# Kernel tuning notes

Measured on AMD Instinct MI355X. Metric: run time of the kernel, lower is better.

Reference implementation:

```python
import jax, jax.numpy as jnp
import numpy as np

B, S, D_IN, E, H, F, O = 32, 1024, 256, 512, 512, 2048, 512


def setup_inputs() -> dict:
    key = jax.random.key(0)
    ks = jax.random.split(key, 10)
    s = 0.02
    return {
        "x": jax.random.normal(ks[0], (B, S, D_IN), dtype=jnp.float32),
        "W_enc": jax.random.normal(ks[1], (D_IN, E), dtype=jnp.float32) * s,
        "b_enc": jnp.zeros((E,), dtype=jnp.float32),
        "W_ih": jax.random.normal(ks[2], (E, 4 * H), dtype=jnp.float32) * s,
        "W_hh": jax.random.normal(ks[3], (H, 4 * H), dtype=jnp.float32) * s,
        "b_lstm": jnp.zeros((4 * H,), dtype=jnp.float32),
        "W1": jax.random.normal(ks[4], (E, F), dtype=jnp.float32) * s,
        "b1": jnp.zeros((F,), dtype=jnp.float32),
        "W2": jax.random.normal(ks[5], (F, O), dtype=jnp.float32) * s,
        "b2": jnp.zeros((O,), dtype=jnp.float32),
    }


def _lstm(xs, W_ih, W_hh, b):
    # xs: [S, B, E] -> outputs [S, B, H], final (h, c) each [B, H]
    h0 = jnp.zeros((xs.shape[1], W_hh.shape[0]), dtype=xs.dtype)
    c0 = jnp.zeros_like(h0)

    def step(carry, x_t):
        h, c = carry
        z = x_t @ W_ih + h @ W_hh + b  # [B, 4H]
        i, f, g, o = jnp.split(z, 4, axis=-1)
        i = jax.nn.sigmoid(i)
        f = jax.nn.sigmoid(f)
        g = jnp.tanh(g)
        o = jax.nn.sigmoid(o)
        c = f * c + i * g
        h = o * jnp.tanh(c)
        return (h, c), h

    (h_n, c_n), ys = jax.lax.scan(step, (h0, c0), xs)
    return ys, h_n, c_n


def reference(x, W_enc, b_enc, W_ih, W_hh, b_lstm, W1, b1, W2, b2):
    # encoder: per-token linear projection, then permute to time-major
    embedded = x @ W_enc + b_enc              # [B, S, E]
    embedded = jnp.transpose(embedded, (1, 0, 2))  # [S, B, E]
    # decoder LSTM over the sequence dimension
    output, h_n, c_n = _lstm(embedded, W_ih, W_hh, b_lstm)
    # per-position 2-layer MLP (vectorized version of the (i,j) loop):
    # fc2(fc1(relu(embedded)))  -- note ReLU is applied BEFORE fc1, and no
    # nonlinearity between fc1 and fc2, matching the torch code.
    embed_out = (jax.nn.relu(embedded) @ W1 + b1) @ W2 + b2  # [S, B, O]
    return output, h_n[None], c_n[None], embed_out
```

## Files before the change

kernel.cpp:

```cpp
#include <hip/hip_runtime.h>
#include <hip/hip_bf16.h>
#include <stdint.h>

typedef uint16_t u16;
typedef uint32_t u32;
typedef unsigned long long u64;
typedef __attribute__((ext_vector_type(8))) short short8;
typedef __attribute__((ext_vector_type(4))) float f32x4;

#define NS 1024

__device__ __forceinline__ float bf2f(u16 v) {
  union { u32 u; float f; } x; x.u = ((u32)v) << 16; return x.f;
}
__device__ __forceinline__ u16 f2bf(float f) {
  union { float f; u32 u; } x; x.f = f;
  u32 r = x.u + 0x7FFFu + ((x.u >> 16) & 1u);
  return (u16)(r >> 16);
}
__device__ __forceinline__ u32 relu2bf(u32 x) {
  u32 kill = (((x >> 15) & 1u) * 0x0000FFFFu) | (((x >> 31) & 1u) * 0xFFFF0000u);
  return x & ~kill;
}
__device__ __forceinline__ f32x4 shfl_x4(f32x4 v, int m) {
  f32x4 r;
  r[0] = __shfl_xor(v[0], m); r[1] = __shfl_xor(v[1], m);
  r[2] = __shfl_xor(v[2], m); r[3] = __shfl_xor(v[3], m);
  return r;
}

__global__ __launch_bounds__(256) void k_cast(const float* __restrict__ in,
                                              u16* __restrict__ out, int n4) {
  int i = blockIdx.x * 256 + threadIdx.x;
  if (i >= n4) return;
  float4 v = ((const float4*)in)[i];
  ushort4 o;
  o.x = f2bf(v.x); o.y = f2bf(v.y); o.z = f2bf(v.z); o.w = f2bf(v.w);
  ((ushort4*)out)[i] = o;
}

__global__ __launch_bounds__(256) void k_transpose(const float* __restrict__ in,
                                                   u16* __restrict__ out,
                                                   int K, int N) {
  __shared__ u16 tile[32][33];
  int k0 = blockIdx.x * 32, n0 = blockIdx.y * 32;
  int tid = threadIdx.x;
#pragma unroll
  for (int i = 0; i < 4; i++) {
    int idx = i * 256 + tid;
    int r = idx >> 5, c = idx & 31;
    tile[r][c] = f2bf(in[(size_t)(k0 + r) * N + n0 + c]);
  }
  __syncthreads();
#pragma unroll
  for (int i = 0; i < 4; i++) {
    int idx = i * 256 + tid;
    int r = idx >> 5, c = idx & 31;
    out[(size_t)(n0 + r) * K + k0 + c] = tile[c][r];
  }
}

template <bool REMAP, bool RELU_A, bool OUTF32>
__global__ __launch_bounds__(256) void k_gemm(const u16* __restrict__ A,
                                              const u16* __restrict__ Bt,
                                              const float* __restrict__ bias,
                                              void* __restrict__ Cout,
                                              int M, int N, int K) {
  __shared__ u16 As[128 * 32];
  __shared__ u16 Bs[128 * 32];
  const int m0 = blockIdx.x * 128, n0 = blockIdx.y * 128;
  const int tid = threadIdx.x;
  const int wave = tid >> 6, lane = tid & 63;
  const int wm = wave >> 1, wn = wave & 1;
  f32x4 acc[4][4] = {};

  for (int kt = 0; kt < K; kt += 32) {
    uint4 av[2], bv[2];
#pragma unroll
    for (int i = 0; i < 2; i++) {
      int idx = i * 256 + tid;
      int r = idx >> 2, ch = idx & 3;
      av[i] = *(const uint4*)(A + (size_t)(m0 + r) * K + kt + ch * 8);
      bv[i] = *(const uint4*)(Bt + (size_t)(n0 + r) * K + kt + ch * 8);
      if (RELU_A) {
        u32* p = (u32*)&av[i];
        p[0] = relu2bf(p[0]); p[1] = relu2bf(p[1]);
        p[2] = relu2bf(p[2]); p[3] = relu2bf(p[3]);
      }
    }
    __syncthreads();
#pragma unroll
    for (int i = 0; i < 2; i++) {
      int idx = i * 256 + tid;
      int r = idx >> 2, ch = idx & 3;
      *(uint4*)(As + r * 32 + ch * 8) = av[i];
      *(uint4*)(Bs + r * 32 + ch * 8) = bv[i];
    }
    __syncthreads();
    short8 af[4], bf[4];
#pragma unroll
    for (int mi = 0; mi < 4; mi++) {
      int row = wm * 64 + mi * 16 + (lane & 15);
      af[mi] = *(const short8*)(As + row * 32 + (lane >> 4) * 8);
    }
#pragma unroll
    for (int ni = 0; ni < 4; ni++) {
      int col = wn * 64 + ni * 16 + (lane & 15);
      bf[ni] = *(const short8*)(Bs + col * 32 + (lane >> 4) * 8);
    }
#pragma unroll
    for (int mi = 0; mi < 4; mi++)
#pragma unroll
      for (int ni = 0; ni < 4; ni++)
        acc[mi][ni] = __builtin_amdgcn_mfma_f32_16x16x32_bf16(af[mi], bf[ni], acc[mi][ni], 0, 0, 0);
  }

#pragma unroll
  for (int mi = 0; mi < 4; mi++)
#pragma unroll
    for (int ni = 0; ni < 4; ni++) {
      int col = n0 + wn * 64 + ni * 16 + (lane & 15);
      float bvad = bias[col];
#pragma unroll
      for (int r = 0; r < 4; r++) {
        int row = m0 + wm * 64 + mi * 16 + (lane >> 4) * 4 + r;
        float v = acc[mi][ni][r] + bvad;
        size_t orow = REMAP ? ((size_t)(row & 1023) * 32 + (size_t)(row >> 10))
                            : (size_t)row;
        if (OUTF32) ((float*)Cout)[orow * N + col] = v;
        else        ((u16*)Cout)[orow * N + col] = f2bf(v);
      }
    }
}

__global__ __launch_bounds__(256, 1) void k_lstm(
    const u16* __restrict__ Whh_t,
    const u16* __restrict__ Wih_t,
    const u16* __restrict__ emb,
    const float* __restrict__ b_lstm,
    u64* __restrict__ hbuf,
    float* __restrict__ out,
    float* __restrict__ hn,
    float* __restrict__ cn)
{
  __shared__ u16 hl[2][32][512];

  const int blk = blockIdx.x;
  const int tid = threadIdx.x;
  const int wave = tid >> 6, lane = tid & 63;
  const int hc0 = blk * 8;
  const int mt = wave >> 1, nt = wave & 1;
  const int g = (lane >> 2) & 3;
  const int j = lane & 3;
  const int arow = mt * 16 + (lane & 15);
  const int crow0 = mt * 16 + (lane >> 4) * 4;
  const int mycol = hc0 + nt * 4 + j;
  const int srow = tid >> 3;
  const int st8 = tid & 7;

  short8 bfh[16], bfx[16];
  {
    int lc = lane & 15;
    int gcol = (lc >> 2) * 512 + hc0 + nt * 4 + (lc & 3);
    const u16* bh = Whh_t + (size_t)gcol * 512 + (lane >> 4) * 8;
    const u16* bx = Wih_t + (size_t)gcol * 512 + (lane >> 4) * 8;
#pragma unroll
    for (int kc = 0; kc < 16; kc++) {
      bfh[kc] = *(const short8*)(bh + kc * 32);
      bfx[kc] = *(const short8*)(bx + kc * 32);
    }
  }
  const float bz = b_lstm[g * 512 + hc0 + nt * 4 + j];

  f32x4 cst = {0.f, 0.f, 0.f, 0.f}, hst = {0.f, 0.f, 0.f, 0.f};

  f32x4 zx0 = {0.f, 0.f, 0.f, 0.f}, zx1 = {0.f, 0.f, 0.f, 0.f};
  {
    const u16* xb = emb + (size_t)arow * 512 + (lane >> 4) * 8;
    short8 af[16];
#pragma unroll
    for (int kc = 0; kc < 16; kc++) af[kc] = *(const short8*)(xb + kc * 32);
#pragma unroll
    for (int kc = 0; kc < 16; kc += 2) {
      zx0 = __builtin_amdgcn_mfma_f32_16x16x32_bf16(af[kc], bfx[kc], zx0, 0, 0, 0);
      zx1 = __builtin_amdgcn_mfma_f32_16x16x32_bf16(af[kc + 1], bfx[kc + 1], zx1, 0, 0, 0);
    }
  }

  char* ldsb = (char*)&hl[0][0][0];

#pragma unroll 1
  for (int s = 0; s < NS; s++) {
    {
      const u64* base = hbuf + (size_t)(s & 1) * 8192 + (size_t)srow * 256;
      const u32 want = (u32)s;
      u32 d[32];
      u32 miss = 0;
#pragma unroll
      for (int k = 0; k < 8; k++)
#pragma unroll
        for (int m = 0; m < 4; m++) {
          int i = k * 4 + m;
          int p = (k * 8 + st8) * 4 + m;
          u64 q = __hip_atomic_load(base + p, __ATOMIC_RELAXED, __HIP_MEMORY_SCOPE_AGENT);
          d[i] = (u32)q;
          if ((u32)(q >> 32) != want) miss |= (1u << i);
        }
      while (__any(miss != 0u)) {
        __builtin_amdgcn_s_sleep(1);
#pragma unroll
        for (int k = 0; k < 8; k++)
#pragma unroll
          for (int m = 0; m < 4; m++) {
            int i = k * 4 + m;
            if (miss & (1u << i)) {
              int p = (k * 8 + st8) * 4 + m;
              u64 q = __hip_atomic_load(base + p, __ATOMIC_RELAXED, __HIP_MEMORY_SCOPE_AGENT);
              if ((u32)(q >> 32) == want) { d[i] = (u32)q; miss &= ~(1u << i); }
            }
          }
      }
      char* lw = ldsb + (size_t)(s & 1) * 32768 + (size_t)srow * 1024;
#pragma unroll
      for (int k = 0; k < 8; k++) {
        uint4 v;
        v.x = d[k * 4]; v.y = d[k * 4 + 1]; v.z = d[k * 4 + 2]; v.w = d[k * 4 + 3];
        int slot = k * 8 + st8;
        int sw = (slot & ~7) | ((slot ^ srow) & 7);
        *(uint4*)(lw + sw * 16) = v;
      }
    }
    __syncthreads();

    f32x4 a0 = zx0, a1 = zx1;
    {
      const char* lr = ldsb + (size_t)(s & 1) * 32768 + (size_t)arow * 1024;
#pragma unroll
      for (int kc = 0; kc < 16; kc += 2) {
        int sl0 = kc * 4 + (lane >> 4);
        int sw0 = (sl0 & ~7) | ((sl0 ^ arow) & 7);
        short8 fa = *(const short8*)(lr + sw0 * 16);
        int sl1 = sl0 + 4;
        int sw1 = (sl1 & ~7) | ((sl1 ^ arow) & 7);
        short8 fb = *(const short8*)(lr + sw1 * 16);
        a0 = __builtin_amdgcn_mfma_f32_16x16x32_bf16(fa, bfh[kc], a0, 0, 0, 0);
        a1 = __builtin_amdgcn_mfma_f32_16x16x32_bf16(fb, bfh[kc + 1], a1, 0, 0, 0);
      }
    }

    f32x4 z0;
#pragma unroll
    for (int r = 0; r < 4; r++) z0[r] = a0[r] + a1[r] + bz;
    f32x4 z1 = shfl_x4(z0, 4);
    f32x4 z2 = shfl_x4(z0, 8);
    f32x4 z3 = shfl_x4(z1, 8);
    f32x4 zi_ = (g == 0) ? z0 : (g == 1) ? z1 : (g == 2) ? z2 : z3;
    f32x4 zf_ = (g == 0) ? z1 : (g == 1) ? z0 : (g == 2) ? z3 : z2;
    f32x4 zg_ = (g == 0) ? z2 : (g == 1) ? z3 : (g == 2) ? z0 : z1;
    f32x4 zo_ = (g == 0) ? z3 : (g == 1) ? z2 : (g == 2) ? z1 : z0;
#pragma unroll
    for (int r = 0; r < 4; r++) {
      float ig = 1.f / (1.f + __expf(-zi_[r]));
      float fg = 1.f / (1.f + __expf(-zf_[r]));
      float gg = tanhf(zg_[r]);
      float og = 1.f / (1.f + __expf(-zo_[r]));
      cst[r] = fg * cst[r] + ig * gg;
      hst[r] = og * tanhf(cst[r]);
    }

    {
      u32 pair[4];
#pragma unroll
      for (int r = 0; r < 4; r++) {
        u16 hb = f2bf(hst[r]);
        u32 nb = (u32)(u16)__shfl_xor((int)hb, 1);
        pair[r] = (u32)hb | (nb << 16);
      }
      if (((lane & 15) & 13) == 0) {
        u64* dst = hbuf + (size_t)((s + 1) & 1) * 8192 + (size_t)crow0 * 256
                 + (size_t)(blk * 4 + nt * 2 + (j >> 1));
        u64 tag = ((u64)(u32)(s + 1)) << 32;
#pragma unroll
        for (int r = 0; r < 4; r++)
          __hip_atomic_store(dst + (size_t)r * 256, tag | pair[r],
                             __ATOMIC_RELAXED, __HIP_MEMORY_SCOPE_AGENT);
      }
    }

    if (g == 0) {
#pragma unroll
      for (int r = 0; r < 4; r++)
        out[((size_t)s * 32 + crow0 + r) * 512 + mycol] = hst[r];
    }

    if (s + 1 < NS) {
      const u16* xb = emb + ((size_t)(s + 1) * 32 + arow) * 512 + (lane >> 4) * 8;
      short8 af2[16];
#pragma unroll
      for (int kc = 0; kc < 16; kc++) af2[kc] = *(const short8*)(xb + kc * 32);
      f32x4 t0 = {0.f, 0.f, 0.f, 0.f}, t1 = {0.f, 0.f, 0.f, 0.f};
#pragma unroll
      for (int kc = 0; kc < 16; kc += 2) {
        t0 = __builtin_amdgcn_mfma_f32_16x16x32_bf16(af2[kc], bfx[kc], t0, 0, 0, 0);
        t1 = __builtin_amdgcn_mfma_f32_16x16x32_bf16(af2[kc + 1], bfx[kc + 1], t1, 0, 0, 0);
      }
      zx0 = t0; zx1 = t1;
    }
  }

  if (g == 0) {
#pragma unroll
    for (int r = 0; r < 4; r++) {
      hn[(size_t)(crow0 + r) * 512 + mycol] = hst[r];
      cn[(size_t)(crow0 + r) * 512 + mycol] = cst[r];
    }
  }
}

extern "C" void kernel_launch(void* const* d_in, const int* in_sizes, int n_in,
                              void* d_out, int out_size, void* d_ws, size_t ws_size,
                              hipStream_t stream) {
  (void)in_sizes; (void)n_in; (void)out_size; (void)ws_size;
  const float* x      = (const float*)d_in[0];
  const float* W_enc  = (const float*)d_in[1];
  const float* b_enc  = (const float*)d_in[2];
  const float* W_ih   = (const float*)d_in[3];
  const float* W_hh   = (const float*)d_in[4];
  const float* b_lstm = (const float*)d_in[5];
  const float* W1     = (const float*)d_in[6];
  const float* b1     = (const float*)d_in[7];
  const float* W2     = (const float*)d_in[8];
  const float* b2     = (const float*)d_in[9];

  char* ws = (char*)d_ws;
  size_t off = 0;
  auto alloc = [&](size_t bytes) -> void* {
    void* p = ws + off;
    off += (bytes + 255) & ~(size_t)255;
    return p;
  };
  u64* hbuf   = (u64*)alloc((size_t)2 * 32 * 256 * 8);
  u16* Wenc_t = (u16*)alloc((size_t)512 * 256 * 2);
  u16* Wih_t  = (u16*)alloc((size_t)2048 * 512 * 2);
  u16* Whh_t  = (u16*)alloc((size_t)2048 * 512 * 2);
  u16* W1_t   = (u16*)alloc((size_t)2048 * 512 * 2);
  u16* W2_t   = (u16*)alloc((size_t)512 * 2048 * 2);
  u16* big    = (u16*)alloc((size_t)8192 * 2048 * 2);
  u16* xbf    = big;
  u16* T      = big;

  float* outp = (float*)d_out;
  float* hnp  = outp + (size_t)16777216;
  float* cnp  = hnp + 16384;
  float* eop  = cnp + 16384;
  u16* emb  = (u16*)(eop + 8388608);

  hipMemsetAsync(hbuf, 0, (size_t)2 * 32 * 256 * 8, stream);

  k_cast<<<8192, 256, 0, stream>>>(x, xbf, 2097152);
  k_transpose<<<dim3(8, 16), 256, 0, stream>>>(W_enc, Wenc_t, 256, 512);
  k_transpose<<<dim3(16, 64), 256, 0, stream>>>(W_ih, Wih_t, 512, 2048);
  k_transpose<<<dim3(16, 64), 256, 0, stream>>>(W_hh, Whh_t, 512, 2048);
  k_transpose<<<dim3(16, 64), 256, 0, stream>>>(W1, W1_t, 512, 2048);
  k_transpose<<<dim3(64, 16), 256, 0, stream>>>(W2, W2_t, 2048, 512);

  k_gemm<true, false, false><<<dim3(256, 4), 256, 0, stream>>>(
      xbf, Wenc_t, b_enc, emb, 32768, 512, 256);

  {
    void* args[] = {(void*)&Whh_t, (void*)&Wih_t, (void*)&emb, (void*)&b_lstm,
                    (void*)&hbuf, (void*)&outp, (void*)&hnp, (void*)&cnp};
    hipError_t cerr = hipLaunchCooperativeKernel((const void*)k_lstm, dim3(64),
                                                 dim3(256), args, 0, stream);
    if (cerr != hipSuccess) {
      (void)hipGetLastError();
      k_lstm<<<dim3(64), dim3(256), 0, stream>>>(Whh_t, Wih_t, emb, b_lstm,
                                                 hbuf, outp, hnp, cnp);
    }
  }

  for (int cch = 0; cch < 4; cch++) {
    const u16* embc = emb + (size_t)cch * 8192 * 512;
    float* eoc = eop + (size_t)cch * 8192 * 512;
    k_gemm<false, true, false><<<dim3(64, 16), 256, 0, stream>>>(
        embc, W1_t, b1, T, 8192, 2048, 512);
    k_gemm<false, false, true><<<dim3(64, 4), 256, 0, stream>>>(
        T, W2_t, b2, eoc, 8192, 512, 2048);
  }
}
```

Before: 6.622 ms.

## Shrink LSTM grid to 16 blocks of 512 threads, each wave covering both batch halves

```diff
diff --git a/kernel.cpp b/kernel.cpp
--- a/kernel.cpp
+++ b/kernel.cpp
@@ -133,7 +133,7 @@
     }
 }
 
-__global__ __launch_bounds__(256, 1) void k_lstm(
+__global__ __launch_bounds__(512, 1) void k_lstm(
     const u16* __restrict__ Whh_t,
     const u16* __restrict__ Wih_t,
     const u16* __restrict__ emb,
@@ -147,16 +147,14 @@
 
   const int blk = blockIdx.x;
   const int tid = threadIdx.x;
-  const int wave = tid >> 6, lane = tid & 63;
-  const int hc0 = blk * 8;
-  const int mt = wave >> 1, nt = wave & 1;
+  const int nt = tid >> 6;
+  const int lane = tid & 63;
+  const int hc0 = blk * 32;
   const int g = (lane >> 2) & 3;
   const int j = lane & 3;
-  const int arow = mt * 16 + (lane & 15);
-  const int crow0 = mt * 16 + (lane >> 4) * 4;
   const int mycol = hc0 + nt * 4 + j;
-  const int srow = tid >> 3;
-  const int st8 = tid & 7;
+  const int srow = tid >> 4;
+  const int st16 = tid & 15;
 
   short8 bfh[16], bfx[16];
   {
@@ -170,21 +168,25 @@
       bfx[kc] = *(const short8*)(bx + kc * 32);
     }
   }
-  const float bz = b_lstm[g * 512 + hc0 + nt * 4 + j];
-
-  f32x4 cst = {0.f, 0.f, 0.f, 0.f}, hst = {0.f, 0.f, 0.f, 0.f};
-
-  f32x4 zx0 = {0.f, 0.f, 0.f, 0.f}, zx1 = {0.f, 0.f, 0.f, 0.f};
-  {
-    const u16* xb = emb + (size_t)arow * 512 + (lane >> 4) * 8;
+  const float bz = b_lstm[g * 512 + mycol];
+
+  f32x4 cst[2] = {}, hst[2] = {};
+  f32x4 zx0[2], zx1[2];
+
+#pragma unroll 2
+  for (int m = 0; m < 2; m++) {
+    const u16* xb = emb + (size_t)(m * 16 + (lane & 15)) * 512 + (lane >> 4) * 8;
     short8 af[16];
 #pragma unroll
     for (int kc = 0; kc < 16; kc++) af[kc] = *(const short8*)(xb + kc * 32);
+    f32x4 t0 = {0.f, 0.f, 0.f, 0.f}, t1 = {0.f, 0.f, 0.f, 0.f};
 #pragma unroll
     for (int kc = 0; kc < 16; kc += 2) {
-      zx0 = __builtin_amdgcn_mfma_f32_16x16x32_bf16(af[kc], bfx[kc], zx0, 0, 0, 0);
-      zx1 = __builtin_amdgcn_mfma_f32_16x16x32_bf16(af[kc + 1], bfx[kc + 1], zx1, 0, 0, 0);
-    }
+      t0 = __builtin_amdgcn_mfma_f32_16x16x32_bf16(af[kc], bfx[kc], t0, 0, 0, 0);
+      t1 = __builtin_amdgcn_mfma_f32_16x16x32_bf16(af[kc + 1], bfx[kc + 1], t1, 0, 0, 0);
+    }
+    zx0[m] = t0; zx1[m] = t1;
+    __builtin_amdgcn_sched_barrier(0);
   }
 
   char* ldsb = (char*)&hl[0][0][0];
@@ -194,14 +196,14 @@
     {
       const u64* base = hbuf + (size_t)(s & 1) * 8192 + (size_t)srow * 256;
       const u32 want = (u32)s;
-      u32 d[32];
+      u32 d[16];
       u32 miss = 0;
 #pragma unroll
-      for (int k = 0; k < 8; k++)
-#pragma unroll
-        for (int m = 0; m < 4; m++) {
-          int i = k * 4 + m;
-          int p = (k * 8 + st8) * 4 + m;
+      for (int k = 0; k < 4; k++)
+#pragma unroll
+        for (int mm = 0; mm < 4; mm++) {
+          int i = k * 4 + mm;
+          int p = (k * 16 + st16) * 4 + mm;
           u64 q = __hip_atomic_load(base + p, __ATOMIC_RELAXED, __HIP_MEMORY_SCOPE_AGENT);
           d[i] = (u32)q;
           if ((u32)(q >> 32) != want) miss |= (1u << i);
@@ -209,12 +211,12 @@
       while (__any(miss != 0u)) {
         __builtin_amdgcn_s_sleep(1);
 #pragma unroll
-        for (int k = 0; k < 8; k++)
-#pragma unroll
-          for (int m = 0; m < 4; m++) {
-            int i = k * 4 + m;
+        for (int k = 0; k < 4; k++)
+#pragma unroll
+          for (int mm = 0; mm < 4; mm++) {
+            int i = k * 4 + mm;
             if (miss & (1u << i)) {
-              int p = (k * 8 + st8) * 4 + m;
+              int p = (k * 16 + st16) * 4 + mm;
               u64 q = __hip_atomic_load(base + p, __ATOMIC_RELAXED, __HIP_MEMORY_SCOPE_AGENT);
               if ((u32)(q >> 32) == want) { d[i] = (u32)q; miss &= ~(1u << i); }
             }
@@ -222,19 +224,22 @@
       }
       char* lw = ldsb + (size_t)(s & 1) * 32768 + (size_t)srow * 1024;
 #pragma unroll
-      for (int k = 0; k < 8; k++) {
+      for (int k = 0; k < 4; k++) {
         uint4 v;
         v.x = d[k * 4]; v.y = d[k * 4 + 1]; v.z = d[k * 4 + 2]; v.w = d[k * 4 + 3];
-        int slot = k * 8 + st8;
+        int slot = k * 16 + st16;
         int sw = (slot & ~7) | ((slot ^ srow) & 7);
         *(uint4*)(lw + sw * 16) = v;
       }
     }
     __syncthreads();
 
-    f32x4 a0 = zx0, a1 = zx1;
-    {
+#pragma unroll 2
+    for (int m = 0; m < 2; m++) {
+      const int arow = m * 16 + (lane & 15);
+      const int crow0 = m * 16 + (lane >> 4) * 4;
       const char* lr = ldsb + (size_t)(s & 1) * 32768 + (size_t)arow * 1024;
+      f32x4 a0 = zx0[m], a1 = zx1[m];
 #pragma unroll
       for (int kc = 0; kc < 16; kc += 2) {
         int sl0 = kc * 4 + (lane >> 4);
@@ -246,73 +251,79 @@
         a0 = __builtin_amdgcn_mfma_f32_16x16x32_bf16(fa, bfh[kc], a0, 0, 0, 0);
         a1 = __builtin_amdgcn_mfma_f32_16x16x32_bf16(fb, bfh[kc + 1], a1, 0, 0, 0);
       }
-    }
-
-    f32x4 z0;
-#pragma unroll
-    for (int r = 0; r < 4; r++) z0[r] = a0[r] + a1[r] + bz;
-    f32x4 z1 = shfl_x4(z0, 4);
-    f32x4 z2 = shfl_x4(z0, 8);
-    f32x4 z3 = shfl_x4(z1, 8);
-    f32x4 zi_ = (g == 0) ? z0 : (g == 1) ? z1 : (g == 2) ? z2 : z3;
-    f32x4 zf_ = (g == 0) ? z1 : (g == 1) ? z0 : (g == 2) ? z3 : z2;
-    f32x4 zg_ = (g == 0) ? z2 : (g == 1) ? z3 : (g == 2) ? z0 : z1;
-    f32x4 zo_ = (g == 0) ? z3 : (g == 1) ? z2 : (g == 2) ? z1 : z0;
-#pragma unroll
-    for (int r = 0; r < 4; r++) {
-      float ig = 1.f / (1.f + __expf(-zi_[r]));
-      float fg = 1.f / (1.f + __expf(-zf_[r]));
-      float gg = tanhf(zg_[r]);
-      float og = 1.f / (1.f + __expf(-zo_[r]));
-      cst[r] = fg * cst[r] + ig * gg;
-      hst[r] = og * tanhf(cst[r]);
-    }
-
-    {
+
+      f32x4 z0;
+#pragma unroll
+      for (int r = 0; r < 4; r++) z0[r] = a0[r] + a1[r] + bz;
+      f32x4 z1 = shfl_x4(z0, 4);
+      f32x4 z2 = shfl_x4(z0, 8);
+      f32x4 z3 = shfl_x4(z1, 8);
+      f32x4 zi_ = (g == 0) ? z0 : (g == 1) ? z1 : (g == 2) ? z2 : z3;
+      f32x4 zf_ = (g == 0) ? z1 : (g == 1) ? z0 : (g == 2) ? z3 : z2;
+      f32x4 zg_ = (g == 0) ? z2 : (g == 1) ? z3 : (g == 2) ? z0 : z1;
+      f32x4 zo_ = (g == 0) ? z3 : (g == 1) ? z2 : (g == 2) ? z1 : z0;
+#pragma unroll
+      for (int r = 0; r < 4; r++) {
+        float ig = 1.f / (1.f + __expf(-zi_[r]));
+        float fg = 1.f / (1.f + __expf(-zf_[r]));
+        float gg = tanhf(zg_[r]);
+        float og = 1.f / (1.f + __expf(-zo_[r]));
+        cst[m][r] = fg * cst[m][r] + ig * gg;
+        hst[m][r] = og * tanhf(cst[m][r]);
+      }
+
       u32 pair[4];
 #pragma unroll
       for (int r = 0; r < 4; r++) {
-        u16 hb = f2bf(hst[r]);
+        u16 hb = f2bf(hst[m][r]);
         u32 nb = (u32)(u16)__shfl_xor((int)hb, 1);
         pair[r] = (u32)hb | (nb << 16);
       }
       if (((lane & 15) & 13) == 0) {
         u64* dst = hbuf + (size_t)((s + 1) & 1) * 8192 + (size_t)crow0 * 256
-                 + (size_t)(blk * 4 + nt * 2 + (j >> 1));
+                 + (size_t)(blk * 16 + nt * 2 + (j >> 1));
         u64 tag = ((u64)(u32)(s + 1)) << 32;
 #pragma unroll
         for (int r = 0; r < 4; r++)
           __hip_atomic_store(dst + (size_t)r * 256, tag | pair[r],
                              __ATOMIC_RELAXED, __HIP_MEMORY_SCOPE_AGENT);
       }
-    }
-
+
+      if (g == 0) {
+#pragma unroll
+        for (int r = 0; r < 4; r++)
+          out[((size_t)s * 32 + crow0 + r) * 512 + mycol] = hst[m][r];
+      }
+    }
+
+    if (s + 1 < NS) {
+#pragma unroll 2
+      for (int m = 0; m < 2; m++) {
+        const u16* xb = emb + ((size_t)(s + 1) * 32 + m * 16 + (lane & 15)) * 512 + (lane >> 4) * 8;
+        short8 af2[16];
+#pragma unroll
+        for (int kc = 0; kc < 16; kc++) af2[kc] = *(const short8*)(xb + kc * 32);
+        f32x4 t0 = {0.f, 0.f, 0.f, 0.f}, t1 = {0.f, 0.f, 0.f, 0.f};
+#pragma unroll
+        for (int kc = 0; kc < 16; kc += 2) {
+          t0 = __builtin_amdgcn_mfma_f32_16x16x32_bf16(af2[kc], bfx[kc], t0, 0, 0, 0);
+          t1 = __builtin_amdgcn_mfma_f32_16x16x32_bf16(af2[kc + 1], bfx[kc + 1], t1, 0, 0, 0);
+        }
+        zx0[m] = t0; zx1[m] = t1;
+        __builtin_amdgcn_sched_barrier(0);
+      }
+    }
+  }
+
+#pragma unroll 2
+  for (int m = 0; m < 2; m++) {
+    const int crow0 = m * 16 + (lane >> 4) * 4;
     if (g == 0) {
 #pragma unroll
-      for (int r = 0; r < 4; r++)
-        out[((size_t)s * 32 + crow0 + r) * 512 + mycol] = hst[r];
-    }
-
-    if (s + 1 < NS) {
-      const u16* xb = emb + ((size_t)(s + 1) * 32 + arow) * 512 + (lane >> 4) * 8;
-      short8 af2[16];
-#pragma unroll
-      for (int kc = 0; kc < 16; kc++) af2[kc] = *(const short8*)(xb + kc * 32);
-      f32x4 t0 = {0.f, 0.f, 0.f, 0.f}, t1 = {0.f, 0.f, 0.f, 0.f};
-#pragma unroll
-      for (int kc = 0; kc < 16; kc += 2) {
-        t0 = __builtin_amdgcn_mfma_f32_16x16x32_bf16(af2[kc], bfx[kc], t0, 0, 0, 0);
-        t1 = __builtin_amdgcn_mfma_f32_16x16x32_bf16(af2[kc + 1], bfx[kc + 1], t1, 0, 0, 0);
-      }
-      zx0 = t0; zx1 = t1;
-    }
-  }
-
-  if (g == 0) {
-#pragma unroll
-    for (int r = 0; r < 4; r++) {
-      hn[(size_t)(crow0 + r) * 512 + mycol] = hst[r];
-      cn[(size_t)(crow0 + r) * 512 + mycol] = cst[r];
+      for (int r = 0; r < 4; r++) {
+        hn[(size_t)(crow0 + r) * 512 + mycol] = hst[m][r];
+        cn[(size_t)(crow0 + r) * 512 + mycol] = cst[m][r];
+      }
     }
   }
 }
@@ -370,11 +381,11 @@
   {
     void* args[] = {(void*)&Whh_t, (void*)&Wih_t, (void*)&emb, (void*)&b_lstm,
                     (void*)&hbuf, (void*)&outp, (void*)&hnp, (void*)&cnp};
-    hipError_t cerr = hipLaunchCooperativeKernel((const void*)k_lstm, dim3(64),
-                                                 dim3(256), args, 0, stream);
+    hipError_t cerr = hipLaunchCooperativeKernel((const void*)k_lstm, dim3(16),
+                                                 dim3(512), args, 0, stream);
     if (cerr != hipSuccess) {
       (void)hipGetLastError();
-      k_lstm<<<dim3(64), dim3(256), 0, stream>>>(Whh_t, Wih_t, emb, b_lstm,
+      k_lstm<<<dim3(16), dim3(512), 0, stream>>>(Whh_t, Wih_t, emb, b_lstm,
                                                  hbuf, outp, hnp, cnp);
     }
   }
```

Result: slower. 12.94 ms (+95.4%).
